# Performance work log

Hardware: AMD Instinct MI355X
Metric: run time of the kernel (lower is better)

Reference implementation:

```python
import jax, jax.numpy as jnp
import numpy as np

DIM = 3072
KV_DIM = 2048
HEADS = 16
DIM_HEAD = 128
INNER = HEADS * DIM_HEAD  # 2048
EPS = 1e-5


def layer_norm(x, g, b):
    mu = jnp.mean(x, axis=-1, keepdims=True)
    var = jnp.var(x, axis=-1, keepdims=True)
    return (x - mu) * jax.lax.rsqrt(var + EPS) * g + b


def setup_inputs() -> dict:
    key = jax.random.key(0)
    ks = jax.random.split(key, 8)
    b, n1, n2 = 2, 2048, 2048
    x = jax.random.normal(ks[0], (b, n1, KV_DIM), dtype=jnp.float32)
    latents = jax.random.normal(ks[1], (b, n2, DIM), dtype=jnp.float32)
    w_q = jax.random.normal(ks[2], (DIM, INNER), dtype=jnp.float32) / np.sqrt(DIM)
    w_kv = jax.random.normal(ks[3], (KV_DIM, 2 * INNER), dtype=jnp.float32) / np.sqrt(KV_DIM)
    w_out = jax.random.normal(ks[4], (INNER, DIM), dtype=jnp.float32) / np.sqrt(INNER)
    ln1_g = jnp.ones((KV_DIM,), jnp.float32)
    ln1_b = jnp.zeros((KV_DIM,), jnp.float32)
    ln2_g = jnp.ones((DIM,), jnp.float32)
    ln2_b = jnp.zeros((DIM,), jnp.float32)
    return {"x": x, "latents": latents, "w_q": w_q, "w_kv": w_kv,
            "w_out": w_out, "ln1_g": ln1_g, "ln1_b": ln1_b,
            "ln2_g": ln2_g, "ln2_b": ln2_b}


def reference(x, latents, w_q, w_kv, w_out, ln1_g, ln1_b, ln2_g, ln2_b):
    b, n2, _ = latents.shape
    xn = layer_norm(x, ln1_g, ln1_b)            # (b, n1, kv_dim)
    ln = layer_norm(latents, ln2_g, ln2_b)      # (b, n2, dim)
    q = ln @ w_q                                # (b, n2, inner)
    kv = xn @ w_kv                              # (b, n1, 2*inner)
    k, v = jnp.split(kv, 2, axis=-1)
    # (b, h, n, d)
    def split_heads(t):
        bs, n, _ = t.shape
        return t.reshape(bs, n, HEADS, DIM_HEAD).transpose(0, 2, 1, 3)
    q, k, v = split_heads(q), split_heads(k), split_heads(v)
    scale = 1.0 / np.sqrt(np.sqrt(DIM_HEAD)).astype(np.float32)
    w = jnp.einsum('bhqd,bhkd->bhqk', q * scale, k * scale)
    w = jax.nn.softmax(w.astype(jnp.float32), axis=-1).astype(q.dtype)
    out = jnp.einsum('bhqk,bhkd->bhqd', w, v)
    out = out.transpose(0, 2, 1, 3).reshape(b, n2, INNER)
    return out @ w_out
```

## Files before the change

### kernel.cpp

```cpp
#include <hip/hip_runtime.h>
#include <type_traits>


using u16 = unsigned short;
using u32 = unsigned int;
typedef __attribute__((ext_vector_type(8))) short short8;
typedef __attribute__((ext_vector_type(4))) float floatx4;
typedef __attribute__((ext_vector_type(4))) unsigned short u16x4;

typedef __attribute__((address_space(1))) const unsigned int gu32;
typedef __attribute__((address_space(3))) unsigned int lu32;

__device__ __forceinline__ void gld16(void* lds, const void* g) {
  __builtin_amdgcn_global_load_lds((gu32*)g, (lu32*)lds, 16, 0, 0);
}

__device__ inline u16 f2bf(float f) {
  u32 u = __float_as_uint(f);
  u32 r = (u + 0x7FFFu + ((u >> 16) & 1u)) >> 16;
  return (u16)r;
}

template <int L>
__global__ __launch_bounds__(256) void ln_cast(const float* __restrict__ in,
                                               const float* __restrict__ gw,
                                               const float* __restrict__ bw,
                                               u16* __restrict__ out) {
  constexpr int C4 = L / 1024;
  const int row = blockIdx.x;
  const int t = threadIdx.x;
  const float* rp = in + (size_t)row * L;
  float4 v[C4];
  float s = 0.f, ss = 0.f;
#pragma unroll
  for (int c = 0; c < C4; ++c) {
    v[c] = *(const float4*)(rp + (c * 256 + t) * 4);
    s += v[c].x + v[c].y + v[c].z + v[c].w;
    ss += v[c].x * v[c].x + v[c].y * v[c].y + v[c].z * v[c].z + v[c].w * v[c].w;
  }
#pragma unroll
  for (int off = 32; off > 0; off >>= 1) {
    s += __shfl_down(s, off);
    ss += __shfl_down(ss, off);
  }
  __shared__ float red[8];
  const int wave = t >> 6, lane = t & 63;
  if (lane == 0) { red[wave] = s; red[4 + wave] = ss; }
  __syncthreads();
  const float tot = red[0] + red[1] + red[2] + red[3];
  const float tss = red[4] + red[5] + red[6] + red[7];
  const float mu = tot * (1.f / L);
  const float rstd = rsqrtf(tss * (1.f / L) - mu * mu + 1e-5f);
  u16* op = out + (size_t)row * L;
#pragma unroll
  for (int c = 0; c < C4; ++c) {
    const int base = (c * 256 + t) * 4;
    float4 gv = *(const float4*)(gw + base);
    float4 bv = *(const float4*)(bw + base);
    u32 p0 = (u32)f2bf((v[c].x - mu) * rstd * gv.x + bv.x) |
             ((u32)f2bf((v[c].y - mu) * rstd * gv.y + bv.y) << 16);
    u32 p1 = (u32)f2bf((v[c].z - mu) * rstd * gv.z + bv.z) |
             ((u32)f2bf((v[c].w - mu) * rstd * gv.w + bv.w) << 16);
    uint2 pk; pk.x = p0; pk.y = p1;
    *(uint2*)(op + base) = pk;
  }
}

__global__ __launch_bounds__(256) void transpose_cast(const float* __restrict__ in,
                                                      u16* __restrict__ out,
                                                      int R, int C) {
  __shared__ u16 tile[32][33];
  const int c0 = blockIdx.x * 32, r0 = blockIdx.y * 32;
  const int x = threadIdx.x, y = threadIdx.y;
#pragma unroll
  for (int j = 0; j < 4; ++j)
    tile[y + 8 * j][x] = f2bf(in[(size_t)(r0 + y + 8 * j) * C + c0 + x]);
  __syncthreads();
#pragma unroll
  for (int j = 0; j < 4; ++j)
    out[(size_t)(c0 + y + 8 * j) * R + r0 + x] = tile[x][y + 8 * j];
}

template <typename OutT>
__global__ __launch_bounds__(256) void gemm_bt(const u16* __restrict__ A,
                                               const u16* __restrict__ Bt,
                                               OutT* __restrict__ C,
                                               int M, int N, int K) {
  __shared__ u16 As[128 * 64];
  __shared__ u16 Bs[128 * 64];
  const int tid = threadIdx.x;
  const int wave = tid >> 6, lane = tid & 63, l16 = lane & 15, quad = lane >> 4;
  const int wm = (wave >> 1) * 64, wn = (wave & 1) * 64;
  const long m0 = (long)blockIdx.y * 128, n0 = (long)blockIdx.x * 128;
  const int srow = tid >> 3;
  const int gc = ((tid & 7) ^ ((tid >> 3) & 7)) * 8;
  const u16* Ag0 = A + (m0 + srow) * (long)K + gc;
  const u16* Bg0 = Bt + (n0 + srow) * (long)K + gc;
  const long rowoff = 32L * K;

  const floatx4 fz = {0.f, 0.f, 0.f, 0.f};
  floatx4 acc[4][4];
#pragma unroll
  for (int i = 0; i < 4; ++i)
#pragma unroll
    for (int j = 0; j < 4; ++j) acc[i][j] = fz;

  for (int k0 = 0; k0 < K; k0 += 64) {
    __syncthreads();
#pragma unroll
    for (int c = 0; c < 4; ++c) {
      gld16(&As[(c * 256 + tid) * 8], Ag0 + c * rowoff + k0);
      gld16(&Bs[(c * 256 + tid) * 8], Bg0 + c * rowoff + k0);
    }
    __syncthreads();
#pragma unroll
    for (int kd = 0; kd < 2; ++kd) {
      const int sw = ((4 * kd + quad) ^ (l16 & 7)) * 8;
      short8 a[4], b[4];
#pragma unroll
      for (int i = 0; i < 4; ++i) a[i] = *(const short8*)&As[(wm + i * 16 + l16) * 64 + sw];
#pragma unroll
      for (int j = 0; j < 4; ++j) b[j] = *(const short8*)&Bs[(wn + j * 16 + l16) * 64 + sw];
#pragma unroll
      for (int i = 0; i < 4; ++i)
#pragma unroll
        for (int j = 0; j < 4; ++j)
          acc[i][j] = __builtin_amdgcn_mfma_f32_16x16x32_bf16(a[i], b[j], acc[i][j], 0, 0, 0);
    }
  }

#pragma unroll
  for (int i = 0; i < 4; ++i)
#pragma unroll
    for (int r = 0; r < 4; ++r) {
      const long row = m0 + wm + i * 16 + quad * 4 + r;
#pragma unroll
      for (int j = 0; j < 4; ++j) {
        const long col = n0 + wn + j * 16 + l16;
        if constexpr (std::is_same<OutT, float>::value)
          C[row * N + col] = acc[i][j][r];
        else
          C[row * N + col] = f2bf(acc[i][j][r]);
      }
    }
}

#define GBAR()                                         \
  do {                                                 \
    asm volatile("" ::: "memory");                     \
    __builtin_amdgcn_s_barrier();                      \
    asm volatile("" ::: "memory");                     \
  } while (0)
#define VMW(N) asm volatile("s_waitcnt vmcnt(" #N ")" ::: "memory")

#define G8_LDA(MH)                                                             \
  {                                                                            \
    const u16* Ab_ = &As[buf][(MH) * 8192 + (wr * 32 + l16) * 64];             \
    _Pragma("unroll") for (int mi = 0; mi < 2; ++mi)                           \
    _Pragma("unroll") for (int ks = 0; ks < 2; ++ks)                           \
      af[mi][ks] = *(const short8*)&Ab_[mi * 1024 + ((4 * ks + quad) ^ swz) * 8]; \
  }
#define G8_LDB(DST, NH)                                                        \
  {                                                                            \
    const u16* Bb_ = &Bs[buf][(NH) * 8192 + (wc * 64 + l16) * 64];             \
    _Pragma("unroll") for (int ni = 0; ni < 4; ++ni)                           \
    _Pragma("unroll") for (int ks = 0; ks < 2; ++ks)                           \
      DST[ni][ks] = *(const short8*)&Bb_[ni * 1024 + ((4 * ks + quad) ^ swz) * 8]; \
  }
#define G8_MFMA(MH, BFX, NH)                                                   \
  __builtin_amdgcn_s_setprio(1);                                               \
  _Pragma("unroll") for (int ks = 0; ks < 2; ++ks)                             \
  _Pragma("unroll") for (int mi = 0; mi < 2; ++mi)                             \
  _Pragma("unroll") for (int ni = 0; ni < 4; ++ni)                             \
    acc[MH][mi][NH][ni] = __builtin_amdgcn_mfma_f32_16x16x32_bf16(             \
        af[mi][ks], BFX[ni][ks], acc[MH][mi][NH][ni], 0, 0, 0);                \
  __builtin_amdgcn_s_setprio(0);

template <typename OutT>
__global__ __launch_bounds__(512, 2) void gemm_bt8(const u16* __restrict__ A,
                                                   const u16* __restrict__ Bt,
                                                   OutT* __restrict__ C,
                                                   int M, int N, int K,
                                                   u16* __restrict__ vT,
                                                   int vcol0) {
  __shared__ u16 As[2][16384];
  __shared__ u16 Bs[2][16384];
  (void)M;
  const int tid = threadIdx.x;
  const int wave = tid >> 6, lane = tid & 63, l16 = lane & 15, quad = lane >> 4;
  const int wr = wave >> 1;
  const int wc = wave & 1;
  const int nwg = gridDim.x * gridDim.y;
  const int bid0 = blockIdx.y * gridDim.x + blockIdx.x;
  const int bid = (bid0 & 7) * (nwg >> 3) + (bid0 >> 3);
  const int bx = bid % gridDim.x, by = bid / gridDim.x;
  const long m0 = (long)by * 256, n0 = (long)bx * 256;

  const int srow = tid >> 3;
  const int gc = ((tid & 7) ^ (srow & 7)) * 8;

  auto stageA = [&](int bufn, int h, int k0) {
#pragma unroll
    for (int c = 0; c < 2; ++c)
      gld16(&As[bufn][h * 8192 + (c * 512 + tid) * 8],
            A + (size_t)(m0 + h * 128 + c * 64 + srow) * K + k0 + gc);
  };
  auto stageB = [&](int bufn, int h, int k0) {
#pragma unroll
    for (int c = 0; c < 2; ++c)
      gld16(&Bs[bufn][h * 8192 + (c * 512 + tid) * 8],
            Bt + (size_t)(n0 + h * 128 + c * 64 + srow) * K + k0 + gc);
  };

  const floatx4 fz = {0.f, 0.f, 0.f, 0.f};
  floatx4 acc[2][2][2][4];
#pragma unroll
  for (int a = 0; a < 2; ++a)
#pragma unroll
    for (int b = 0; b < 2; ++b)
#pragma unroll
      for (int c = 0; c < 2; ++c)
#pragma unroll
        for (int d = 0; d < 4; ++d) acc[a][b][c][d] = fz;

  short8 af[2][2], bf0[4][2], bf1[4][2];
  const int swz = l16 & 7;

  stageA(0, 0, 0);
  stageB(0, 0, 0);
  stageB(0, 1, 0);
  stageA(0, 1, 0);
  VMW(4);
  GBAR();

  const int NT = K >> 6;
  for (int t = 0; t < NT; ++t) {
    const int buf = t & 1;
    const int kn = (t + 1) << 6;
    const bool pre = (t + 1 < NT);

    G8_LDA(0);
    G8_LDB(bf0, 0);
    if (pre) stageA(buf ^ 1, 0, kn);
    GBAR();
    G8_MFMA(0, bf0, 0);
    if (pre) { VMW(4); } else { VMW(2); }
    GBAR();

    G8_LDB(bf1, 1);
    if (pre) stageB(buf ^ 1, 0, kn);
    GBAR();
    G8_MFMA(0, bf1, 1);
    if (pre) { VMW(4); } else { VMW(0); }
    GBAR();

    G8_LDA(1);
    if (pre) stageB(buf ^ 1, 1, kn);
    GBAR();
    G8_MFMA(1, bf0, 0);
    GBAR();

    if (pre) stageA(buf ^ 1, 1, kn);
    GBAR();
    G8_MFMA(1, bf1, 1);
    if (pre) { VMW(4); }
    GBAR();
  }

  bool vpath = false;
  if constexpr (std::is_same<OutT, u16>::value) vpath = (n0 >= vcol0);
  if (vpath) {
    u16* tl = (u16*)&As[0][0];
#pragma unroll
    for (int mh = 0; mh < 2; ++mh)
#pragma unroll
      for (int nh = 0; nh < 2; ++nh) {
        const long R0 = m0 + mh * 128;
        const long bb = R0 >> 11, nn0 = R0 & 2047;
        const long hh = (n0 + nh * 128 - vcol0) >> 7;
        __syncthreads();
        const int dl0 = wc * 64 + l16;
        const int nl0 = wr * 32 + quad * 4;
#pragma unroll
        for (int mi = 0; mi < 2; ++mi)
#pragma unroll
          for (int ni = 0; ni < 4; ++ni) {
            u16x4 pk;
#pragma unroll
            for (int rr = 0; rr < 4; ++rr) pk[rr] = f2bf(acc[mh][mi][nh][ni][rr]);
            *(u16x4*)&tl[(dl0 + ni * 16) * 136 + nl0 + mi * 16] = pk;
          }
        __syncthreads();
        const int d = tid >> 2, sg = (tid & 3) * 32;
        u16* gp = &vT[(((bb * 16 + hh) * 128 + d) << 11) + nn0 + sg];
        const u16* lp = &tl[d * 136 + sg];
#pragma unroll
        for (int j = 0; j < 4; ++j)
          *(short8*)&gp[j * 8] = *(const short8*)&lp[j * 8];
      }
  } else {
#pragma unroll
    for (int mh = 0; mh < 2; ++mh)
#pragma unroll
      for (int mi = 0; mi < 2; ++mi)
#pragma unroll
        for (int rr = 0; rr < 4; ++rr) {
          const long row = m0 + mh * 128 + wr * 32 + mi * 16 + quad * 4 + rr;
#pragma unroll
          for (int nh = 0; nh < 2; ++nh)
#pragma unroll
            for (int ni = 0; ni < 4; ++ni) {
              const long col = n0 + nh * 128 + wc * 64 + ni * 16 + l16;
              if constexpr (std::is_same<OutT, float>::value)
                C[row * N + col] = acc[mh][mi][nh][ni][rr];
              else
                C[row * N + col] = f2bf(acc[mh][mi][nh][ni][rr]);
            }
        }
  }
}

#undef G8_LDA
#undef G8_LDB
#undef G8_MFMA

__global__ __launch_bounds__(256, 2) void flash_attn(const u16* __restrict__ Q,
                                                     const u16* __restrict__ KV,
                                                     const u16* __restrict__ VT,
                                                     u16* __restrict__ O) {
  __shared__ u16 Ks[2][64 * 128];
  __shared__ u16 Vs[2][128 * 64];
  __shared__ u16 Ps[4][32 * 64];
  const int tid = threadIdx.x;
  const int wave = tid >> 6, lane = tid & 63, l16 = lane & 15, quad = lane >> 4;
  const int d = blockIdx.x;
  const int bh = (d & 7) * 4 + ((d >> 3) & 3);
  const int qt = d >> 5;
  const int b = bh >> 4, h = bh & 15;
  const u16* Qb = Q + (size_t)b * 2048 * 2048 + h * 128;
  const u16* Kb = KV + (size_t)b * 2048 * 4096 + h * 128;
  const u16* Vb = VT + (size_t)bh * 128 * 2048;
  u16* Ob = O + (size_t)b * 2048 * 2048 + h * 128;
  const int q0 = qt * 128 + wave * 32;

  short8 qf[2][4];
#pragma unroll
  for (int t = 0; t < 2; ++t)
#pragma unroll
    for (int kd = 0; kd < 4; ++kd)
      qf[t][kd] = *(const short8*)&Qb[(size_t)(q0 + t * 16 + l16) * 2048 + kd * 32 + quad * 8];

  short8 onesf;
  {
    union { short8 s; u32 w[4]; } uo;
    const u32 o = (l16 == 0) ? 0x3F803F80u : 0u;
#pragma unroll
    for (int i = 0; i < 4; ++i) uo.w[i] = o;
    onesf = uo.s;
  }

  const floatx4 fz = {0.f, 0.f, 0.f, 0.f};
  floatx4 oacc[2][9];
  float m[2][4];
#pragma unroll
  for (int t = 0; t < 2; ++t) {
#pragma unroll
    for (int jd = 0; jd < 9; ++jd) oacc[t][jd] = fz;
#pragma unroll
    for (int r = 0; r < 4; ++r) m[t][r] = -1e30f;
  }

  u16* Psw = Ps[wave];
  const float sc2 = 0.12751775f;
  const float THR2 = 11.5416f;

  auto stage = [&](int buf, int kv0) {
#pragma unroll
    for (int c = 0; c < 4; ++c) {
      const int li = c * 256 + tid;
      const int krow = li >> 4, kdb = (li & 15) ^ (krow & 15);
      gld16(&Ks[buf][li * 8], Kb + (size_t)(kv0 + krow) * 4096 + kdb * 8);
      const int vrow = li >> 3, vdb = (li & 7) ^ (vrow & 7);
      gld16(&Vs[buf][li * 8], Vb + (size_t)vrow * 2048 + kv0 + vdb * 8);
    }
  };

  stage(0, 0);
  int cur = 0;

  for (int kt = 0; kt < 32; ++kt) {
    __syncthreads();
    if (kt < 31) stage(cur ^ 1, (kt + 1) * 64);
    const u16* Kc = Ks[cur];
    const u16* Vc = Vs[cur];

    floatx4 sacc[2][4];
#pragma unroll
    for (int t = 0; t < 2; ++t)
#pragma unroll
      for (int jn = 0; jn < 4; ++jn) sacc[t][jn] = fz;
    __builtin_amdgcn_s_setprio(1);
#pragma unroll
    for (int jn = 0; jn < 4; ++jn)
#pragma unroll
      for (int kd = 0; kd < 4; ++kd) {
        short8 kb = *(const short8*)&Kc[(jn * 16 + l16) * 128 + ((4 * kd + quad) ^ l16) * 8];
        sacc[0][jn] = __builtin_amdgcn_mfma_f32_16x16x32_bf16(qf[0][kd], kb, sacc[0][jn], 0, 0, 0);
        sacc[1][jn] = __builtin_amdgcn_mfma_f32_16x16x32_bf16(qf[1][kd], kb, sacc[1][jn], 0, 0, 0);
      }
    __builtin_amdgcn_s_setprio(0);

#pragma unroll
    for (int t = 0; t < 2; ++t) {
#pragma unroll
      for (int r = 0; r < 4; ++r) {
        float mx = fmaxf(fmaxf(sacc[t][0][r], sacc[t][1][r]),
                         fmaxf(sacc[t][2][r], sacc[t][3][r]));
#pragma unroll
        for (int off = 8; off > 0; off >>= 1) mx = fmaxf(mx, __shfl_xor(mx, off, 16));
        const float mxs = sc2 * mx;
        if (!__all(mxs - m[t][r] <= THR2)) {
          const float mnew = fmaxf(m[t][r], mxs);
          const float alpha = __builtin_amdgcn_exp2f(m[t][r] - mnew);
          m[t][r] = mnew;
#pragma unroll
          for (int jd = 0; jd < 9; ++jd) oacc[t][jd][r] *= alpha;
        }
        const float mrow = m[t][r];
        const int q = t * 16 + quad * 4 + r;
        const int mask = (q & 7) ^ (q >> 3);
        u16* prow = &Psw[q * 64 + (l16 & 7)];
#pragma unroll
        for (int jn = 0; jn < 4; ++jn) {
          const float p = __builtin_amdgcn_exp2f(fmaf(sc2, sacc[t][jn][r], -mrow));
          const int slot = (2 * jn + (l16 >> 3)) ^ mask;
          prow[slot * 8] = f2bf(p);
        }
      }
    }

    const int pmask0 = (l16 & 7) ^ (l16 >> 3);
    const int pmask1 = (l16 & 7) ^ (2 + (l16 >> 3));
    __builtin_amdgcn_s_setprio(1);
#pragma unroll
    for (int kk = 0; kk < 2; ++kk) {
      const int chunk = 4 * kk + quad;
      short8 pf0 = *(const short8*)&Psw[(l16) * 64 + (chunk ^ pmask0) * 8];
      short8 pf1 = *(const short8*)&Psw[(16 + l16) * 64 + (chunk ^ pmask1) * 8];
#pragma unroll
      for (int jd = 0; jd < 8; ++jd) {
        short8 vb = *(const short8*)&Vc[(jd * 16 + l16) * 64 + (chunk ^ (l16 & 7)) * 8];
        oacc[0][jd] = __builtin_amdgcn_mfma_f32_16x16x32_bf16(pf0, vb, oacc[0][jd], 0, 0, 0);
        oacc[1][jd] = __builtin_amdgcn_mfma_f32_16x16x32_bf16(pf1, vb, oacc[1][jd], 0, 0, 0);
      }
      oacc[0][8] = __builtin_amdgcn_mfma_f32_16x16x32_bf16(pf0, onesf, oacc[0][8], 0, 0, 0);
      oacc[1][8] = __builtin_amdgcn_mfma_f32_16x16x32_bf16(pf1, onesf, oacc[1][8], 0, 0, 0);
    }
    __builtin_amdgcn_s_setprio(0);
    cur ^= 1;
  }

#pragma unroll
  for (int t = 0; t < 2; ++t)
#pragma unroll
    for (int r = 0; r < 4; ++r) {
      const float l = __shfl(oacc[t][8][r], lane & 48);
      const float inv = 1.f / l;
      const size_t row = q0 + t * 16 + quad * 4 + r;
#pragma unroll
      for (int jd = 0; jd < 8; ++jd)
        Ob[row * 2048 + jd * 16 + l16] = f2bf(oacc[t][jd][r] * inv);
    }
}

extern "C" void kernel_launch(void* const* d_in, const int* in_sizes, int n_in,
                              void* d_out, int out_size, void* d_ws, size_t ws_size,
                              hipStream_t stream) {
  const float* x       = (const float*)d_in[0];
  const float* latents = (const float*)d_in[1];
  const float* w_q     = (const float*)d_in[2];
  const float* w_kv    = (const float*)d_in[3];
  const float* w_out   = (const float*)d_in[4];
  const float* ln1_g   = (const float*)d_in[5];
  const float* ln1_b   = (const float*)d_in[6];
  const float* ln2_g   = (const float*)d_in[7];
  const float* ln2_b   = (const float*)d_in[8];

  char* ws = (char*)d_ws;
  u16* xn    = (u16*)(ws);
  u16* lnl   = (u16*)(ws + 16777216);
  u16* wqT   = (u16*)(ws + 41943040);
  u16* wkvT  = (u16*)(ws + 54525952);
  u16* woutT = (u16*)(ws + 71303168);
  u16* qb    = (u16*)(ws + 83886080);
  u16* kvb   = (u16*)(ws + 100663296);
  u16* vTb   = lnl;
  u16* attn  = xn;

  ln_cast<2048><<<dim3(4096), 256, 0, stream>>>(x, ln1_g, ln1_b, xn);
  ln_cast<3072><<<dim3(4096), 256, 0, stream>>>(latents, ln2_g, ln2_b, lnl);

  transpose_cast<<<dim3(64, 96), dim3(32, 8), 0, stream>>>(w_q, wqT, 3072, 2048);
  transpose_cast<<<dim3(128, 64), dim3(32, 8), 0, stream>>>(w_kv, wkvT, 2048, 4096);
  transpose_cast<<<dim3(96, 64), dim3(32, 8), 0, stream>>>(w_out, woutT, 2048, 3072);

  gemm_bt<u16><<<dim3(16, 32), 256, 0, stream>>>(lnl, wqT, qb, 4096, 2048, 3072);
  gemm_bt8<u16><<<dim3(16, 16), 512, 0, stream>>>(xn, wkvT, kvb, 4096, 4096, 2048,
                                                  vTb, 2048);

  flash_attn<<<dim3(512), 256, 0, stream>>>(qb, kvb, vTb, attn);

  gemm_bt8<float><<<dim3(12, 16), 512, 0, stream>>>(attn, woutT, (float*)d_out,
                                                    4096, 3072, 2048, nullptr,
                                                    1 << 30);
}
```

Baseline: 506.0 us.

## Merge LN and transpose launches, replace Q-projection GEMM with pipelined kernel

Merges the two layer-norm launches into one grid and the three weight transpose-cast launches into one grid, which cuts launch overhead and tail effects. Replaces the simple single-buffered 128x128 Q-projection GEMM with a 512-thread 256x128 kernel. The new kernel double-buffers LDS via async global-to-LDS loads, overlaps loads with MFMA, raises wave priority around MFMA blocks, and swizzles block order for cache locality. It uses more LDS and registers per block, which can reduce occupancy.

```diff
diff --git a/kernel.cpp b/kernel.cpp
--- a/kernel.cpp
+++ b/kernel.cpp
@@ -22,12 +22,11 @@
 }
 
 template <int L>
-__global__ __launch_bounds__(256) void ln_cast(const float* __restrict__ in,
-                                               const float* __restrict__ gw,
-                                               const float* __restrict__ bw,
-                                               u16* __restrict__ out) {
+__device__ __forceinline__ void ln_body(const float* __restrict__ in,
+                                        const float* __restrict__ gw,
+                                        const float* __restrict__ bw,
+                                        u16* __restrict__ out, int row) {
   constexpr int C4 = L / 1024;
-  const int row = blockIdx.x;
   const int t = threadIdx.x;
   const float* rp = in + (size_t)row * L;
   float4 v[C4];
@@ -66,11 +65,32 @@
   }
 }
 
-__global__ __launch_bounds__(256) void transpose_cast(const float* __restrict__ in,
-                                                      u16* __restrict__ out,
-                                                      int R, int C) {
+__global__ __launch_bounds__(256) void ln_cast2(const float* __restrict__ x,
+                                                const float* __restrict__ lat,
+                                                const float* __restrict__ g1,
+                                                const float* __restrict__ b1,
+                                                const float* __restrict__ g2,
+                                                const float* __restrict__ b2,
+                                                u16* __restrict__ xn,
+                                                u16* __restrict__ lnl) {
+  const int bid = blockIdx.x;
+  if (bid < 4096) ln_body<2048>(x, g1, b1, xn, bid);
+  else            ln_body<3072>(lat, g2, b2, lnl, bid - 4096);
+}
+
+__global__ __launch_bounds__(256) void transpose_cast3(const float* __restrict__ wq,
+                                                       const float* __restrict__ wkv,
+                                                       const float* __restrict__ wout,
+                                                       u16* __restrict__ oq,
+                                                       u16* __restrict__ okv,
+                                                       u16* __restrict__ oout) {
   __shared__ u16 tile[32][33];
-  const int c0 = blockIdx.x * 32, r0 = blockIdx.y * 32;
+  const int bid = blockIdx.x;
+  const float* in; u16* out; int R, C, gx, tb;
+  if (bid < 6144)       { in = wq;   out = oq;   R = 3072; C = 2048; gx = 64;  tb = bid; }
+  else if (bid < 14336) { in = wkv;  out = okv;  R = 2048; C = 4096; gx = 128; tb = bid - 6144; }
+  else                  { in = wout; out = oout; R = 2048; C = 3072; gx = 96;  tb = bid - 14336; }
+  const int c0 = (tb % gx) * 32, r0 = (tb / gx) * 32;
   const int x = threadIdx.x, y = threadIdx.y;
 #pragma unroll
   for (int j = 0; j < 4; ++j)
@@ -79,70 +99,6 @@
 #pragma unroll
   for (int j = 0; j < 4; ++j)
     out[(size_t)(c0 + y + 8 * j) * R + r0 + x] = tile[x][y + 8 * j];
-}
-
-template <typename OutT>
-__global__ __launch_bounds__(256) void gemm_bt(const u16* __restrict__ A,
-                                               const u16* __restrict__ Bt,
-                                               OutT* __restrict__ C,
-                                               int M, int N, int K) {
-  __shared__ u16 As[128 * 64];
-  __shared__ u16 Bs[128 * 64];
-  const int tid = threadIdx.x;
-  const int wave = tid >> 6, lane = tid & 63, l16 = lane & 15, quad = lane >> 4;
-  const int wm = (wave >> 1) * 64, wn = (wave & 1) * 64;
-  const long m0 = (long)blockIdx.y * 128, n0 = (long)blockIdx.x * 128;
-  const int srow = tid >> 3;
-  const int gc = ((tid & 7) ^ ((tid >> 3) & 7)) * 8;
-  const u16* Ag0 = A + (m0 + srow) * (long)K + gc;
-  const u16* Bg0 = Bt + (n0 + srow) * (long)K + gc;
-  const long rowoff = 32L * K;
-
-  const floatx4 fz = {0.f, 0.f, 0.f, 0.f};
-  floatx4 acc[4][4];
-#pragma unroll
-  for (int i = 0; i < 4; ++i)
-#pragma unroll
-    for (int j = 0; j < 4; ++j) acc[i][j] = fz;
-
-  for (int k0 = 0; k0 < K; k0 += 64) {
-    __syncthreads();
-#pragma unroll
-    for (int c = 0; c < 4; ++c) {
-      gld16(&As[(c * 256 + tid) * 8], Ag0 + c * rowoff + k0);
-      gld16(&Bs[(c * 256 + tid) * 8], Bg0 + c * rowoff + k0);
-    }
-    __syncthreads();
-#pragma unroll
-    for (int kd = 0; kd < 2; ++kd) {
-      const int sw = ((4 * kd + quad) ^ (l16 & 7)) * 8;
-      short8 a[4], b[4];
-#pragma unroll
-      for (int i = 0; i < 4; ++i) a[i] = *(const short8*)&As[(wm + i * 16 + l16) * 64 + sw];
-#pragma unroll
-      for (int j = 0; j < 4; ++j) b[j] = *(const short8*)&Bs[(wn + j * 16 + l16) * 64 + sw];
-#pragma unroll
-      for (int i = 0; i < 4; ++i)
-#pragma unroll
-        for (int j = 0; j < 4; ++j)
-          acc[i][j] = __builtin_amdgcn_mfma_f32_16x16x32_bf16(a[i], b[j], acc[i][j], 0, 0, 0);
-    }
-  }
-
-#pragma unroll
-  for (int i = 0; i < 4; ++i)
-#pragma unroll
-    for (int r = 0; r < 4; ++r) {
-      const long row = m0 + wm + i * 16 + quad * 4 + r;
-#pragma unroll
-      for (int j = 0; j < 4; ++j) {
-        const long col = n0 + wn + j * 16 + l16;
-        if constexpr (std::is_same<OutT, float>::value)
-          C[row * N + col] = acc[i][j][r];
-        else
-          C[row * N + col] = f2bf(acc[i][j][r]);
-      }
-    }
 }
 
 #define GBAR()                                         \
@@ -152,6 +108,131 @@
     asm volatile("" ::: "memory");                     \
   } while (0)
 #define VMW(N) asm volatile("s_waitcnt vmcnt(" #N ")" ::: "memory")
+
+__global__ __launch_bounds__(512, 2) void gemm_bt4(const u16* __restrict__ A,
+                                                   const u16* __restrict__ Bt,
+                                                   u16* __restrict__ C,
+                                                   int M, int N, int K) {
+  __shared__ u16 As[2][2][8192];
+  __shared__ u16 Bs[2][8192];
+  (void)M;
+  const int tid = threadIdx.x;
+  const int wave = tid >> 6, lane = tid & 63, l16 = lane & 15, quad = lane >> 4;
+  const int wr = wave >> 1;
+  const int wc = wave & 1;
+  const int nwg = gridDim.x * gridDim.y;
+  const int bid0 = blockIdx.y * gridDim.x + blockIdx.x;
+  const int bid = (bid0 & 7) * (nwg >> 3) + (bid0 >> 3);
+  const int bx = bid % gridDim.x, by = bid / gridDim.x;
+  const long m0 = (long)by * 256, n0 = (long)bx * 128;
+
+  const int srow = tid >> 3;
+  const int gc = ((tid & 7) ^ (srow & 7)) * 8;
+
+  auto stageAh = [&](int bufn, int mh, int k0) {
+#pragma unroll
+    for (int c = 0; c < 2; ++c)
+      gld16(&As[bufn][mh][(c * 512 + tid) * 8],
+            A + (size_t)(m0 + mh * 128 + c * 64 + srow) * K + k0 + gc);
+  };
+  auto stageBh = [&](int bufn, int k0) {
+#pragma unroll
+    for (int c = 0; c < 2; ++c)
+      gld16(&Bs[bufn][(c * 512 + tid) * 8],
+            Bt + (size_t)(n0 + c * 64 + srow) * K + k0 + gc);
+  };
+
+  const floatx4 fz = {0.f, 0.f, 0.f, 0.f};
+  floatx4 acc[2][2][4];
+#pragma unroll
+  for (int a = 0; a < 2; ++a)
+#pragma unroll
+    for (int b = 0; b < 2; ++b)
+#pragma unroll
+      for (int c = 0; c < 4; ++c) acc[a][b][c] = fz;
+
+  short8 af[2][2], bf[4][2];
+  const int swz = l16 & 7;
+
+  stageAh(0, 0, 0);
+  stageBh(0, 0);
+  stageAh(0, 1, 0);
+  VMW(2);
+  GBAR();
+
+  const int NT = K >> 6;
+  for (int t = 0; t < NT; ++t) {
+    const int buf = t & 1;
+    const int kn = (t + 1) << 6;
+    const bool pre = (t + 1 < NT);
+
+    {
+      const u16* Ab_ = &As[buf][0][(wr * 32 + l16) * 64];
+#pragma unroll
+      for (int mi = 0; mi < 2; ++mi)
+#pragma unroll
+        for (int ks = 0; ks < 2; ++ks)
+          af[mi][ks] = *(const short8*)&Ab_[mi * 1024 + ((4 * ks + quad) ^ swz) * 8];
+      const u16* Bb_ = &Bs[buf][(wc * 64 + l16) * 64];
+#pragma unroll
+      for (int ni = 0; ni < 4; ++ni)
+#pragma unroll
+        for (int ks = 0; ks < 2; ++ks)
+          bf[ni][ks] = *(const short8*)&Bb_[ni * 1024 + ((4 * ks + quad) ^ swz) * 8];
+    }
+    if (pre) { stageAh(buf ^ 1, 0, kn); stageBh(buf ^ 1, kn); }
+    GBAR();
+    __builtin_amdgcn_s_setprio(1);
+#pragma unroll
+    for (int ks = 0; ks < 2; ++ks)
+#pragma unroll
+      for (int mi = 0; mi < 2; ++mi)
+#pragma unroll
+        for (int ni = 0; ni < 4; ++ni)
+          acc[0][mi][ni] = __builtin_amdgcn_mfma_f32_16x16x32_bf16(
+              af[mi][ks], bf[ni][ks], acc[0][mi][ni], 0, 0, 0);
+    __builtin_amdgcn_s_setprio(0);
+    if (pre) { VMW(4); } else { VMW(0); }
+    GBAR();
+
+    {
+      const u16* Ab_ = &As[buf][1][(wr * 32 + l16) * 64];
+#pragma unroll
+      for (int mi = 0; mi < 2; ++mi)
+#pragma unroll
+        for (int ks = 0; ks < 2; ++ks)
+          af[mi][ks] = *(const short8*)&Ab_[mi * 1024 + ((4 * ks + quad) ^ swz) * 8];
+    }
+    if (pre) stageAh(buf ^ 1, 1, kn);
+    GBAR();
+    __builtin_amdgcn_s_setprio(1);
+#pragma unroll
+    for (int ks = 0; ks < 2; ++ks)
+#pragma unroll
+      for (int mi = 0; mi < 2; ++mi)
+#pragma unroll
+        for (int ni = 0; ni < 4; ++ni)
+          acc[1][mi][ni] = __builtin_amdgcn_mfma_f32_16x16x32_bf16(
+              af[mi][ks], bf[ni][ks], acc[1][mi][ni], 0, 0, 0);
+    __builtin_amdgcn_s_setprio(0);
+    if (pre) { VMW(2); }
+    GBAR();
+  }
+
+#pragma unroll
+  for (int mh = 0; mh < 2; ++mh)
+#pragma unroll
+    for (int mi = 0; mi < 2; ++mi)
+#pragma unroll
+      for (int rr = 0; rr < 4; ++rr) {
+        const long row = m0 + mh * 128 + wr * 32 + mi * 16 + quad * 4 + rr;
+#pragma unroll
+        for (int ni = 0; ni < 4; ++ni) {
+          const long col = n0 + wc * 64 + ni * 16 + l16;
+          C[row * N + col] = f2bf(acc[mh][mi][ni][rr]);
+        }
+      }
+}
 
 #define G8_LDA(MH)                                                             \
   {                                                                            \
@@ -497,14 +578,13 @@
   u16* vTb   = lnl;
   u16* attn  = xn;
 
-  ln_cast<2048><<<dim3(4096), 256, 0, stream>>>(x, ln1_g, ln1_b, xn);
-  ln_cast<3072><<<dim3(4096), 256, 0, stream>>>(latents, ln2_g, ln2_b, lnl);
-
-  transpose_cast<<<dim3(64, 96), dim3(32, 8), 0, stream>>>(w_q, wqT, 3072, 2048);
-  transpose_cast<<<dim3(128, 64), dim3(32, 8), 0, stream>>>(w_kv, wkvT, 2048, 4096);
-  transpose_cast<<<dim3(96, 64), dim3(32, 8), 0, stream>>>(w_out, woutT, 2048, 3072);
-
-  gemm_bt<u16><<<dim3(16, 32), 256, 0, stream>>>(lnl, wqT, qb, 4096, 2048, 3072);
+  ln_cast2<<<dim3(8192), 256, 0, stream>>>(x, latents, ln1_g, ln1_b,
+                                           ln2_g, ln2_b, xn, lnl);
+
+  transpose_cast3<<<dim3(20480), dim3(32, 8), 0, stream>>>(w_q, w_kv, w_out,
+                                                           wqT, wkvT, woutT);
+
+  gemm_bt4<<<dim3(16, 16), 512, 0, stream>>>(lnl, wqT, qb, 4096, 2048, 3072);
   gemm_bt8<u16><<<dim3(16, 16), 512, 0, stream>>>(xn, wkvT, kvb, 4096, 4096, 2048,
                                                   vTb, 2048);
 
```

After: 494.0 us. 1.02x faster.
